# Optimization experiments

Measured on AMD Instinct MI355X. Metric: run time of the kernel, lower is better.

## Reference

```python
import jax, jax.numpy as jnp
import numpy as np

N, D = 8192, 1024
MAX_REP = 8

def setup_inputs() -> dict:
    key = jax.random.key(0)
    k1, k2 = jax.random.split(key)
    encoder_h = jax.random.normal(k1, (N, D), dtype=jnp.float32)
    repeats = jax.random.randint(k2, (N,), 0, MAX_REP, dtype=jnp.int32)
    return {"encoder_h": encoder_h, "repeats": repeats}

def reference(encoder_h, repeats):
    # Variable-length repeat_interleave along axis 0.
    # Equivalent to tf tile+sequence_mask+boolean_mask+reshape in the original,
    # but expressed as a single cumsum-index gather (no max_repeat-sized blowup).
    repeats = repeats.astype(jnp.int32)
    total = int(jnp.sum(repeats))  # dynamic output length (data-dependent)
    csum = jnp.cumsum(repeats)                     # [N]
    # row index for each output slot: searchsorted maps output position -> source row
    idx = jnp.searchsorted(csum, jnp.arange(total, dtype=jnp.int32), side='right')  # [total]
    return encoder_h[idx]                          # [total, D]
```

## Files before the change

kernel.cpp:

```cpp
#include <hip/hip_runtime.h>


#define SCAN_THREADS 1024
#define ELEMS_PER_THREAD 8
#define ROWS_PER_BLOCK 4

__global__ __launch_bounds__(SCAN_THREADS)
void scan_scatter_kernel(const int* __restrict__ repeats,
                         int* __restrict__ idx_map, int n) {
    __shared__ int tmp[SCAN_THREADS];
    const int t = threadIdx.x;
    const int base = t * ELEMS_PER_THREAD;
    int vals[ELEMS_PER_THREAD];
    int s = 0;
#pragma unroll
    for (int j = 0; j < ELEMS_PER_THREAD; ++j) {
        const int idx = base + j;
        const int v = (idx < n) ? repeats[idx] : 0;
        vals[j] = v;
        s += v;
    }
    tmp[t] = s;
    __syncthreads();
    for (int off = 1; off < SCAN_THREADS; off <<= 1) {
        const int v = (t >= off) ? tmp[t - off] : 0;
        __syncthreads();
        tmp[t] += v;
        __syncthreads();
    }
    int run = tmp[t] - s;
#pragma unroll
    for (int j = 0; j < ELEMS_PER_THREAD; ++j) {
        const int src_row = base + j;
        const int r = vals[j];
        for (int k = 0; k < r; ++k) {
            idx_map[run + k] = src_row;
        }
        run += r;
    }
}

__global__ __launch_bounds__(256)
void gather_rows_kernel(const float4* __restrict__ h,
                        const int* __restrict__ idx_map,
                        float4* __restrict__ out,
                        int total_rows, int d4 ) {
    const int row0 = blockIdx.x * ROWS_PER_BLOCK;
    int srcs[ROWS_PER_BLOCK];
#pragma unroll
    for (int r = 0; r < ROWS_PER_BLOCK; ++r) {
        const int row = row0 + r;
        srcs[r] = (row < total_rows) ? idx_map[row] : 0;
    }
#pragma unroll
    for (int r = 0; r < ROWS_PER_BLOCK; ++r) {
        const int row = row0 + r;
        if (row >= total_rows) return;
        const float4* __restrict__ src = h + (size_t)srcs[r] * d4;
        float4* __restrict__ dst = out + (size_t)row * d4;
        for (int i = threadIdx.x; i < d4; i += blockDim.x) {
            dst[i] = src[i];
        }
    }
}

extern "C" void kernel_launch(void* const* d_in, const int* in_sizes, int n_in,
                              void* d_out, int out_size, void* d_ws, size_t ws_size,
                              hipStream_t stream) {
    const float* encoder_h = (const float*)d_in[0];
    const int*   repeats   = (const int*)d_in[1];
    float*       out       = (float*)d_out;

    const int n = in_sizes[1];
    const int d = in_sizes[0] / n;
    const int total_rows = out_size / d;

    int* idx_map = (int*)d_ws;

    scan_scatter_kernel<<<1, SCAN_THREADS, 0, stream>>>(repeats, idx_map, n);

    const int nblocks = (total_rows + ROWS_PER_BLOCK - 1) / ROWS_PER_BLOCK;
    gather_rows_kernel<<<nblocks, 256, 0, stream>>>(
        (const float4*)encoder_h, idx_map, (float4*)out, total_rows, d / 4);
}
```

Before: 160.9 us.

## Use wave-shuffle scan, LDS index staging, u16 indices and nontemporal gather stores

Replaces the shared-memory Hillis-Steele scan with a wave-level shuffle scan plus a small per-wave prefix pass, cutting barriers. The scattered index writes go to LDS first and are then copied out coalesced, using 16-bit indices. The gather kernel handles 8 rows per block and writes output with nontemporal stores so the write-once output bypasses cache. The u16 indices assume fewer than 65536 source rows, and the LDS path assumes total_rows fits in 64KB; otherwise a global fallback runs.

After: 163.3 us. About the same (+1.5%).

```diff
diff --git a/kernel.cpp b/kernel.cpp
--- a/kernel.cpp
+++ b/kernel.cpp
@@ -1,16 +1,24 @@
 #include <hip/hip_runtime.h>
 
 
+typedef float nfloat4 __attribute__((ext_vector_type(4)));
+
 #define SCAN_THREADS 1024
 #define ELEMS_PER_THREAD 8
-#define ROWS_PER_BLOCK 4
+#define ROWS_PER_BLOCK 8
 
 __global__ __launch_bounds__(SCAN_THREADS)
-void scan_scatter_kernel(const int* __restrict__ repeats,
-                         int* __restrict__ idx_map, int n) {
-    __shared__ int tmp[SCAN_THREADS];
+void scan_scatter_lds_kernel(const int* __restrict__ repeats,
+                             unsigned short* __restrict__ idx_map,
+                             int n, int total_rows) {
+    extern __shared__ unsigned short lds_idx[];
+    __shared__ int wsum[SCAN_THREADS / 64];
+
     const int t = threadIdx.x;
+    const int lane = t & 63;
+    const int wave = t >> 6;
     const int base = t * ELEMS_PER_THREAD;
+
     int vals[ELEMS_PER_THREAD];
     int s = 0;
 #pragma unroll
@@ -20,46 +28,111 @@
         vals[j] = v;
         s += v;
     }
-    tmp[t] = s;
+    int isum = s;
+#pragma unroll
+    for (int off = 1; off < 64; off <<= 1) {
+        const int v = __shfl_up(isum, off, 64);
+        if (lane >= off) isum += v;
+    }
+    if (lane == 63) wsum[wave] = isum;
     __syncthreads();
-    for (int off = 1; off < SCAN_THREADS; off <<= 1) {
-        const int v = (t >= off) ? tmp[t - off] : 0;
-        __syncthreads();
-        tmp[t] += v;
-        __syncthreads();
+    if (t == 0) {
+        int acc = 0;
+#pragma unroll
+        for (int w = 0; w < SCAN_THREADS / 64; ++w) {
+            const int v = wsum[w];
+            wsum[w] = acc;
+            acc += v;
+        }
     }
-    int run = tmp[t] - s;
+    __syncthreads();
+    int run = wsum[wave] + isum - s;
+
 #pragma unroll
     for (int j = 0; j < ELEMS_PER_THREAD; ++j) {
         const int src_row = base + j;
         const int r = vals[j];
         for (int k = 0; k < r; ++k) {
-            idx_map[run + k] = src_row;
+            lds_idx[run + k] = (unsigned short)src_row;
+        }
+        run += r;
+    }
+    __syncthreads();
+
+    for (int p = t; p < total_rows; p += SCAN_THREADS) {
+        idx_map[p] = lds_idx[p];
+    }
+}
+
+__global__ __launch_bounds__(SCAN_THREADS)
+void scan_scatter_global_kernel(const int* __restrict__ repeats,
+                                unsigned short* __restrict__ idx_map, int n) {
+    __shared__ int wsum[SCAN_THREADS / 64];
+    const int t = threadIdx.x;
+    const int lane = t & 63;
+    const int wave = t >> 6;
+    const int base = t * ELEMS_PER_THREAD;
+
+    int vals[ELEMS_PER_THREAD];
+    int s = 0;
+#pragma unroll
+    for (int j = 0; j < ELEMS_PER_THREAD; ++j) {
+        const int idx = base + j;
+        const int v = (idx < n) ? repeats[idx] : 0;
+        vals[j] = v;
+        s += v;
+    }
+    int isum = s;
+#pragma unroll
+    for (int off = 1; off < 64; off <<= 1) {
+        const int v = __shfl_up(isum, off, 64);
+        if (lane >= off) isum += v;
+    }
+    if (lane == 63) wsum[wave] = isum;
+    __syncthreads();
+    if (t == 0) {
+        int acc = 0;
+#pragma unroll
+        for (int w = 0; w < SCAN_THREADS / 64; ++w) {
+            const int v = wsum[w];
+            wsum[w] = acc;
+            acc += v;
+        }
+    }
+    __syncthreads();
+    int run = wsum[wave] + isum - s;
+#pragma unroll
+    for (int j = 0; j < ELEMS_PER_THREAD; ++j) {
+        const int src_row = base + j;
+        const int r = vals[j];
+        for (int k = 0; k < r; ++k) {
+            idx_map[run + k] = (unsigned short)src_row;
         }
         run += r;
     }
 }
 
 __global__ __launch_bounds__(256)
-void gather_rows_kernel(const float4* __restrict__ h,
-                        const int* __restrict__ idx_map,
-                        float4* __restrict__ out,
+void gather_rows_kernel(const nfloat4* __restrict__ h,
+                        const unsigned short* __restrict__ idx_map,
+                        nfloat4* __restrict__ out,
                         int total_rows, int d4 ) {
     const int row0 = blockIdx.x * ROWS_PER_BLOCK;
     int srcs[ROWS_PER_BLOCK];
 #pragma unroll
     for (int r = 0; r < ROWS_PER_BLOCK; ++r) {
         const int row = row0 + r;
-        srcs[r] = (row < total_rows) ? idx_map[row] : 0;
+        srcs[r] = (row < total_rows) ? (int)idx_map[row] : 0;
     }
 #pragma unroll
     for (int r = 0; r < ROWS_PER_BLOCK; ++r) {
         const int row = row0 + r;
         if (row >= total_rows) return;
-        const float4* __restrict__ src = h + (size_t)srcs[r] * d4;
-        float4* __restrict__ dst = out + (size_t)row * d4;
+        const nfloat4* __restrict__ src = h + (size_t)srcs[r] * d4;
+        nfloat4* __restrict__ dst = out + (size_t)row * d4;
         for (int i = threadIdx.x; i < d4; i += blockDim.x) {
-            dst[i] = src[i];
+            const nfloat4 v = src[i];
+            __builtin_nontemporal_store(v, &dst[i]);
         }
     }
 }
@@ -75,11 +148,18 @@
     const int d = in_sizes[0] / n;
     const int total_rows = out_size / d;
 
-    int* idx_map = (int*)d_ws;
+    unsigned short* idx_map = (unsigned short*)d_ws;
 
-    scan_scatter_kernel<<<1, SCAN_THREADS, 0, stream>>>(repeats, idx_map, n);
+    const size_t lds_bytes = ((size_t)total_rows * 2 + 3) & ~(size_t)3;
+    if (lds_bytes <= 64 * 1024) {
+        scan_scatter_lds_kernel<<<1, SCAN_THREADS, lds_bytes, stream>>>(
+            repeats, idx_map, n, total_rows);
+    } else {
+        scan_scatter_global_kernel<<<1, SCAN_THREADS, 0, stream>>>(
+            repeats, idx_map, n);
+    }
 
     const int nblocks = (total_rows + ROWS_PER_BLOCK - 1) / ROWS_PER_BLOCK;
     gather_rows_kernel<<<nblocks, 256, 0, stream>>>(
-        (const float4*)encoder_h, idx_map, (float4*)out, total_rows, d / 4);
+        (const nfloat4*)encoder_h, idx_map, (nfloat4*)out, total_rows, d / 4);
 }
```
